# Performance work log

Measured on AMD Instinct MI355X. Metric: run time of the kernel, lower is better.

## Reference

```python
import jax, jax.numpy as jnp
import numpy as np


def setup_inputs() -> dict:
    key0 = jax.random.key(0)
    kq, kk, kv = jax.random.split(key0, 3)
    B, S, E = 4, 2048, 1024
    query = jax.random.normal(kq, (B, S, E), dtype=jnp.float32)
    key = jax.random.normal(kk, (B, S, E), dtype=jnp.float32)
    value = jax.random.normal(kv, (B, S, E), dtype=jnp.float32)
    attn_mask = jnp.zeros((B, S, S), dtype=jnp.float32)
    return {"query": query, "key": key, "value": value, "attn_mask": attn_mask}


def reference(query, key, value, attn_mask):
    # qk = Q K^T / sqrt(E) + mask; softmax over last dim; dropout is
    # identity in eval mode (reference baseline); out = attn @ V.
    E = query.shape[-1]
    scale = 1.0 / jnp.sqrt(jnp.asarray(E, dtype=query.dtype))
    qk = jnp.einsum("bqe,bke->bqk", query, key) * scale + attn_mask
    attn = jax.nn.softmax(qk, axis=-1)
    out = jnp.einsum("bqk,bke->bqe", attn, value)
    return out
```

## Files before the change

kernel.cpp:

```cpp
#include <hip/hip_runtime.h>
#include <stdint.h>
#include <math.h>

typedef unsigned short u16;
typedef short bf16x8 __attribute__((ext_vector_type(8)));
typedef unsigned short u16x8 __attribute__((ext_vector_type(8)));
typedef unsigned short u16x4 __attribute__((ext_vector_type(4)));
typedef float f32x4 __attribute__((ext_vector_type(4)));

typedef __attribute__((address_space(1))) const void gvoid;
typedef __attribute__((address_space(3))) void lvoid;

#define LOG2E 1.4426950408889634f

__device__ __forceinline__ float bf2f(u16 u) {
  union { unsigned int i; float f; } v; v.i = ((unsigned int)u) << 16; return v.f;
}
__device__ __forceinline__ u16 f2bf(float f) {
  union { float ff; unsigned int i; } v; v.ff = f;
  unsigned int x = v.i;
  return (u16)((x + 0x7FFFu + ((x >> 16) & 1u)) >> 16);
}

__global__ __launch_bounds__(256)
void cvt2_f32_bf16(const float* __restrict__ s0, u16* __restrict__ d0,
                   const float* __restrict__ s1, u16* __restrict__ d1, long n)
{
  const long nb = n / 2048;
  const float* src = (blockIdx.x < nb) ? s0 : s1;
  u16* dst         = (blockIdx.x < nb) ? d0 : d1;
  const long bid   = (blockIdx.x < nb) ? blockIdx.x : (blockIdx.x - nb);
  long i = (bid * 256 + threadIdx.x) * 8;
  if (i + 8 > n) return;
  f32x4 a = *(const f32x4*)&src[i];
  f32x4 b = *(const f32x4*)&src[i + 4];
  u16x8 o;
#pragma unroll
  for (int j = 0; j < 4; j++) { o[j] = f2bf(a[j]); o[4 + j] = f2bf(b[j]); }
  *(u16x8*)&dst[i] = o;
}

__global__ __launch_bounds__(256)
void cvt_f32_bf16(const float* __restrict__ src, u16* __restrict__ dst, long n)
{
  long i = ((long)blockIdx.x * 256 + threadIdx.x) * 8;
  if (i + 8 > n) return;
  f32x4 a = *(const f32x4*)&src[i];
  f32x4 b = *(const f32x4*)&src[i + 4];
  u16x8 o;
#pragma unroll
  for (int j = 0; j < 4; j++) { o[j] = f2bf(a[j]); o[4 + j] = f2bf(b[j]); }
  *(u16x8*)&dst[i] = o;
}

__global__ __launch_bounds__(256)
void transcvt_v(const float* __restrict__ V, u16* __restrict__ VT, int S, int E)
{
  __shared__ u16 t[64][72];
  const int b = blockIdx.z;
  const float* Vb = V + (long)b * S * E;
  u16* VTb = VT + (long)b * S * E;
  const int k0 = blockIdx.x * 64, n0 = blockIdx.y * 64;
  const int tid = threadIdx.x;
#pragma unroll
  for (int p = 0; p < 2; p++) {
    int kk = p * 32 + (tid >> 3);
    int nn = (tid & 7) * 8;
    f32x4 a = *(const f32x4*)&Vb[(long)(k0 + kk) * E + n0 + nn];
    f32x4 c = *(const f32x4*)&Vb[(long)(k0 + kk) * E + n0 + nn + 4];
#pragma unroll
    for (int j = 0; j < 4; j++) { t[nn + j][kk] = f2bf(a[j]); t[nn + 4 + j][kk] = f2bf(c[j]); }
  }
  __syncthreads();
#pragma unroll
  for (int p = 0; p < 2; p++) {
    int nn = p * 32 + (tid >> 3);
    int kk = (tid & 7) * 8;
    u16x8 u;
#pragma unroll
    for (int j = 0; j < 8; j++) u[j] = t[nn][kk + j];
    *(u16x8*)&VTb[(long)(n0 + nn) * S + k0 + kk] = u;
  }
}

template<int HASMASK, int COUT>
__global__ __launch_bounds__(256, 3)
void gemm_bt_fast(const u16* __restrict__ A, int lda, long aRowOff,
                  const u16* __restrict__ B, int ldb, long bBatchStride,
                  void* __restrict__ Cp, int ldc, long cRowOff,
                  const float* __restrict__ maskf,
                  int K, float scale, long g0, int S)
{
  const int tid  = threadIdx.x;
  const int lane = tid & 63;
  const int wave = tid >> 6;
  const long gTile = g0 + (long)blockIdx.y * 128;
  const int  bidx  = (int)(gTile / S);
  const int  nTile = blockIdx.x * 128;

  __shared__ u16 As[128][32];
  __shared__ u16 Bs[128][32];

  const u16* Ab = A + (gTile - aRowOff) * (long)lda;
  const u16* Bb = B + (long)bidx * bBatchStride + (long)nTile * ldb;

  const int qm = (wave >> 1) * 64;
  const int qn = (wave & 1) * 64;
  const int lm  = lane & 15;
  const int lkB = (lane >> 4) * 16;

  const int sr = lane >> 2;
  const int sc = (lane & 3) * 8;

  f32x4 acc[4][4];
#pragma unroll
  for (int i = 0; i < 4; i++)
#pragma unroll
    for (int j = 0; j < 4; j++) acc[i][j] = (f32x4){0.f, 0.f, 0.f, 0.f};

  for (int k0 = 0; k0 < K; k0 += 32) {
#pragma unroll
    for (int p = 0; p < 2; p++) {
      const int chunk = wave * 2 + p;
      const int r = chunk * 16 + sr;
      __builtin_amdgcn_global_load_lds(
          (gvoid*)&Ab[(long)r * lda + k0 + sc],
          (lvoid*)((char*)&As[0][0] + chunk * 1024),
          16, 0, 0);
      __builtin_amdgcn_global_load_lds(
          (gvoid*)&Bb[(long)r * ldb + k0 + sc],
          (lvoid*)((char*)&Bs[0][0] + chunk * 1024),
          16, 0, 0);
    }
    __syncthreads();

    bf16x8 af[4], bfr[4];
#pragma unroll
    for (int rt = 0; rt < 4; rt++)
      af[rt] = *(const bf16x8*)((const char*)&As[qm + rt * 16 + lm][0] + lkB);
#pragma unroll
    for (int ct = 0; ct < 4; ct++)
      bfr[ct] = *(const bf16x8*)((const char*)&Bs[qn + ct * 16 + lm][0] + lkB);

#pragma unroll
    for (int rt = 0; rt < 4; rt++)
#pragma unroll
      for (int ct = 0; ct < 4; ct++)
        acc[rt][ct] = __builtin_amdgcn_mfma_f32_16x16x32_bf16(af[rt], bfr[ct], acc[rt][ct], 0, 0, 0);
    __syncthreads();
  }

  const int lr = (lane >> 4) * 4;
#pragma unroll
  for (int rt = 0; rt < 4; rt++) {
#pragma unroll
    for (int ct = 0; ct < 4; ct++) {
      long gr = gTile + qm + rt * 16 + lr;
      int  cc = nTile + qn + ct * 16 + lm;
#pragma unroll
      for (int i = 0; i < 4; i++) {
        float v = acc[rt][ct][i] * scale;
        if (HASMASK) v += maskf[(gr + i) * (long)ldc + cc];
        if (COUT == 0)
          ((u16*)Cp)[(gr + i - cRowOff) * (long)ldc + cc] = f2bf(v);
        else
          ((float*)Cp)[(gr + i - cRowOff) * (long)ldc + cc] = v;
      }
    }
  }
}

template<int ASRC, int BSRC, int BMODE, int HASMASK, int COUT>
__global__ __launch_bounds__(256, 2)
void gemm_bt(const void* __restrict__ Ap, int lda, long aRowOff,
             const void* __restrict__ Bp, int ldb, long bBatchStride,
             void* __restrict__ Cp, int ldc, long cRowOff,
             const float* __restrict__ maskf,
             int K, float scale, long g0, int S)
{
  const int tid  = threadIdx.x;
  const int lane = tid & 63;
  const int wave = tid >> 6;
  const long gTile = g0 + (long)blockIdx.y * 128;
  const int  b     = (int)(gTile / S);
  const int  nTile = blockIdx.x * 128;

  __shared__ u16 As[128][40];
  __shared__ u16 Bs[128][40];

  const int qm = (wave >> 1) * 64;
  const int qn = (wave & 1) * 64;

  f32x4 acc[4][4];
#pragma unroll
  for (int i = 0; i < 4; i++)
#pragma unroll
    for (int j = 0; j < 4; j++) acc[i][j] = (f32x4){0.f, 0.f, 0.f, 0.f};

  const u16*   Ab = (const u16*)Ap   + (gTile - aRowOff) * (long)lda;
  const float* Af = (const float*)Ap + (gTile - aRowOff) * (long)lda;
  const u16*   Bb = (const u16*)Bp   + (long)b * bBatchStride;
  const float* Bf = (const float*)Bp + (long)b * bBatchStride;

  const int lm = lane & 15;
  const int lk = (lane >> 4) * 8;

  for (int k0 = 0; k0 < K; k0 += 32) {
    if (ASRC == 0) {
      int srow = tid >> 2, scol = (tid & 3) * 8;
#pragma unroll
      for (int p = 0; p < 2; p++) {
        int r = p * 64 + srow;
        *(u16x8*)&As[r][scol] = *(const u16x8*)&Ab[(long)r * lda + k0 + scol];
      }
    } else {
      int srow = tid >> 3, scol = (tid & 7) * 4;
#pragma unroll
      for (int p = 0; p < 4; p++) {
        int r = p * 32 + srow;
        f32x4 a = *(const f32x4*)&Af[(long)r * lda + k0 + scol];
        u16x4 o;
#pragma unroll
        for (int j = 0; j < 4; j++) o[j] = f2bf(a[j]);
        *(u16x4*)&As[r][scol] = o;
      }
    }
    if (BMODE == 0) {
      if (BSRC == 0) {
        int srow = tid >> 2, scol = (tid & 3) * 8;
#pragma unroll
        for (int p = 0; p < 2; p++) {
          int r = p * 64 + srow;
          *(u16x8*)&Bs[r][scol] = *(const u16x8*)&Bb[(long)(nTile + r) * ldb + k0 + scol];
        }
      } else {
        int srow = tid >> 3, scol = (tid & 7) * 4;
#pragma unroll
        for (int p = 0; p < 4; p++) {
          int r = p * 32 + srow;
          f32x4 a = *(const f32x4*)&Bf[(long)(nTile + r) * ldb + k0 + scol];
          u16x4 o;
#pragma unroll
          for (int j = 0; j < 4; j++) o[j] = f2bf(a[j]);
          *(u16x4*)&Bs[r][scol] = o;
        }
      }
    }
    __syncthreads();

    bf16x8 af[4], bfr[4];
#pragma unroll
    for (int rt = 0; rt < 4; rt++)
      af[rt] = *(const bf16x8*)&As[qm + rt * 16 + lm][lk];
    if (BMODE == 0) {
#pragma unroll
      for (int ct = 0; ct < 4; ct++)
        bfr[ct] = *(const bf16x8*)&Bs[qn + ct * 16 + lm][lk];
    } else {
#pragma unroll
      for (int ct = 0; ct < 4; ct++) {
        const float* vp = Bf + (long)(k0 + lk) * ldb + nTile + qn + ct * 16 + lm;
#pragma unroll
        for (int j = 0; j < 8; j++) bfr[ct][j] = (short)f2bf(vp[(long)j * ldb]);
      }
    }
#pragma unroll
    for (int rt = 0; rt < 4; rt++)
#pragma unroll
      for (int ct = 0; ct < 4; ct++)
        acc[rt][ct] = __builtin_amdgcn_mfma_f32_16x16x32_bf16(af[rt], bfr[ct], acc[rt][ct], 0, 0, 0);
    __syncthreads();
  }

  const int lr = (lane >> 4) * 4;
#pragma unroll
  for (int rt = 0; rt < 4; rt++) {
#pragma unroll
    for (int ct = 0; ct < 4; ct++) {
      long gr = gTile + qm + rt * 16 + lr;
      int  cc = nTile + qn + ct * 16 + lm;
#pragma unroll
      for (int i = 0; i < 4; i++) {
        float v = acc[rt][ct][i] * scale;
        if (HASMASK) v += maskf[(gr + i) * (long)ldc + cc];
        if (COUT == 0)
          ((u16*)Cp)[(gr + i - cRowOff) * (long)ldc + cc] = f2bf(v);
        else
          ((float*)Cp)[(gr + i - cRowOff) * (long)ldc + cc] = v;
      }
    }
  }
}

template<int HASM>
__global__ __launch_bounds__(256)
void softmax_rows(u16* __restrict__ Sbuf, const float* __restrict__ maskf, int ncols)
{
  const long row = blockIdx.x;
  u16* rp = Sbuf + row * (long)ncols;
  const int tid = threadIdx.x;

  u16x8 u = *(const u16x8*)&rp[tid * 8];
  float x[8];
  if (HASM) {
    const float* mp = maskf + row * (long)ncols + tid * 8;
    f32x4 ma = *(const f32x4*)&mp[0];
    f32x4 mb = *(const f32x4*)&mp[4];
#pragma unroll
    for (int i = 0; i < 4; i++) { x[i] = bf2f(u[i]) + ma[i]; x[4 + i] = bf2f(u[4 + i]) + mb[i]; }
  } else {
#pragma unroll
    for (int i = 0; i < 8; i++) x[i] = bf2f(u[i]);
  }
  float m = -3.0e38f;
#pragma unroll
  for (int i = 0; i < 8; i++) m = fmaxf(m, x[i]);
#pragma unroll
  for (int off = 32; off; off >>= 1) m = fmaxf(m, __shfl_xor(m, off, 64));
  __shared__ float redm[4];
  if ((tid & 63) == 0) redm[tid >> 6] = m;
  __syncthreads();
  m = fmaxf(fmaxf(redm[0], redm[1]), fmaxf(redm[2], redm[3]));

  float e[8];
  float s = 0.f;
#pragma unroll
  for (int i = 0; i < 8; i++) { e[i] = exp2f((x[i] - m) * LOG2E); s += e[i]; }
#pragma unroll
  for (int off = 32; off; off >>= 1) s += __shfl_xor(s, off, 64);
  __shared__ float reds[4];
  if ((tid & 63) == 0) reds[tid >> 6] = s;
  __syncthreads();
  s = reds[0] + reds[1] + reds[2] + reds[3];

  float inv = 1.0f / s;
  u16x8 o;
#pragma unroll
  for (int i = 0; i < 8; i++) o[i] = f2bf(e[i] * inv);
  *(u16x8*)&rp[tid * 8] = o;
}

extern "C" void kernel_launch(void* const* d_in, const int* in_sizes, int n_in,
                              void* d_out, int out_size, void* d_ws, size_t ws_size,
                              hipStream_t stream)
{
  const float* Q    = (const float*)d_in[0];
  const float* Km   = (const float*)d_in[1];
  const float* V    = (const float*)d_in[2];
  const float* mask = (const float*)d_in[3];
  float* out = (float*)d_out;

  const long qsz = in_sizes[0];
  const long msz = in_sizes[3];
  const long E = 1024;
  const long S = (msz / qsz) * E;
  const long B = qsz / (S * E);
  const long G = B * S;
  const float scale = 1.0f / sqrtf((float)E);

  const size_t mergedBytes = (size_t)(2 * qsz) * 2 + (size_t)G * S * 2;
  if (ws_size >= mergedBytes) {
    char* w = (char*)d_ws;
    u16* Qb   = (u16*)w;
    u16* Kb   = (u16*)(w + (size_t)qsz * 2);
    u16* Sbuf = (u16*)(w + (size_t)(2 * qsz) * 2);
    u16* VTb  = Qb;

    cvt2_f32_bf16<<<dim3((unsigned)(2 * qsz / 2048)), 256, 0, stream>>>(
        Q, Qb, Km, Kb, qsz);

    gemm_bt_fast<0, 0><<<dim3(S / 128, G / 128), 256, 0, stream>>>(
        Qb, (int)E, 0L, Kb, (int)E, S * E,
        Sbuf, (int)S, 0L, nullptr, (int)E, scale, 0L, (int)S);

    softmax_rows<1><<<dim3((unsigned)G), 256, 0, stream>>>(Sbuf, mask, (int)S);

    transcvt_v<<<dim3(S / 64, E / 64, B), 256, 0, stream>>>(V, VTb, (int)S, (int)E);

    gemm_bt_fast<0, 1><<<dim3(E / 128, G / 128), 256, 0, stream>>>(
        Sbuf, (int)S, 0L, VTb, (int)S, E * S,
        out, (int)E, 0L, nullptr, (int)S, 1.0f, 0L, (int)S);
    return;
  }

  const size_t convBytes = (size_t)(3 * qsz) * 2;
  const size_t rowBytes  = (size_t)S * 2;
  char* w = (char*)d_ws;
  size_t avail = ws_size;
  const bool haveConv = (ws_size >= convBytes + 128 * rowBytes);

  u16 *Qb = nullptr, *Kb = nullptr, *VTb = nullptr;
  if (haveConv) {
    Qb  = (u16*)w;              w += (size_t)qsz * 2;
    Kb  = (u16*)w;              w += (size_t)qsz * 2;
    VTb = (u16*)w;              w += (size_t)qsz * 2;
    avail -= convBytes;
  }
  long Rmax = (long)((avail / rowBytes) / 128) * 128;
  if (Rmax > G) Rmax = G;
  if (Rmax < 128) Rmax = 128;
  u16* Sbuf = (u16*)w;

  if (haveConv) {
    cvt_f32_bf16<<<dim3((unsigned)(qsz / 2048)), 256, 0, stream>>>(Q, Qb, qsz);
    cvt_f32_bf16<<<dim3((unsigned)(qsz / 2048)), 256, 0, stream>>>(Km, Kb, qsz);
    transcvt_v<<<dim3(S / 64, E / 64, B), 256, 0, stream>>>(V, VTb, (int)S, (int)E);
  }

  for (long g0 = 0; g0 < G; g0 += Rmax) {
    const long R = (G - g0 < Rmax) ? (G - g0) : Rmax;
    if (haveConv) {
      gemm_bt_fast<1, 0><<<dim3(S / 128, R / 128), 256, 0, stream>>>(
          Qb, (int)E, 0L, Kb, (int)E, S * E,
          Sbuf, (int)S, g0, mask, (int)E, scale, g0, (int)S);
    } else {
      gemm_bt<1, 1, 0, 1, 0><<<dim3(S / 128, R / 128), 256, 0, stream>>>(
          Q, (int)E, 0L, Km, (int)E, S * E,
          Sbuf, (int)S, g0, mask, (int)E, scale, g0, (int)S);
    }
    softmax_rows<0><<<dim3(R), 256, 0, stream>>>(Sbuf, nullptr, (int)S);
    if (haveConv) {
      gemm_bt_fast<0, 1><<<dim3(E / 128, R / 128), 256, 0, stream>>>(
          Sbuf, (int)S, g0, VTb, (int)S, E * S,
          out, (int)E, 0L, nullptr, (int)S, 1.0f, g0, (int)S);
    } else {
      gemm_bt<0, 1, 1, 0, 1><<<dim3(E / 128, R / 128), 256, 0, stream>>>(
          Sbuf, (int)S, g0, V, (int)E, S * E,
          out, (int)E, 0L, nullptr, (int)S, 1.0f, g0, (int)S);
    }
  }
}
```

Baseline: 279.2 us.

## Double-buffer LDS tiles in gemm_bt_fast to overlap global loads with MFMA

```diff
diff --git a/kernel.cpp b/kernel.cpp
--- a/kernel.cpp
+++ b/kernel.cpp
@@ -98,8 +98,8 @@
   const int  bidx  = (int)(gTile / S);
   const int  nTile = blockIdx.x * 128;
 
-  __shared__ u16 As[128][32];
-  __shared__ u16 Bs[128][32];
+  __shared__ u16 As[2][128][32];
+  __shared__ u16 Bs[2][128][32];
 
   const u16* Ab = A + (gTile - aRowOff) * (long)lda;
   const u16* Bb = B + (long)bidx * bBatchStride + (long)nTile * ldb;
@@ -107,7 +107,7 @@
   const int qm = (wave >> 1) * 64;
   const int qn = (wave & 1) * 64;
   const int lm  = lane & 15;
-  const int lkB = (lane >> 4) * 16;
+  const int lk8 = (lane >> 4) * 8;
 
   const int sr = lane >> 2;
   const int sc = (lane & 3) * 8;
@@ -118,36 +118,56 @@
 #pragma unroll
     for (int j = 0; j < 4; j++) acc[i][j] = (f32x4){0.f, 0.f, 0.f, 0.f};
 
-  for (int k0 = 0; k0 < K; k0 += 32) {
+  auto STAGE = [&](int buf, int t) {
 #pragma unroll
     for (int p = 0; p < 2; p++) {
       const int chunk = wave * 2 + p;
-      const int r = chunk * 16 + sr;
+      const int rr = chunk * 16 + sr;
+      const int gc = t * 32 + sc;
       __builtin_amdgcn_global_load_lds(
-          (gvoid*)&Ab[(long)r * lda + k0 + sc],
-          (lvoid*)((char*)&As[0][0] + chunk * 1024),
+          (gvoid*)&Ab[(long)rr * lda + gc],
+          (lvoid*)((char*)&As[buf][0][0] + chunk * 1024),
           16, 0, 0);
       __builtin_amdgcn_global_load_lds(
-          (gvoid*)&Bb[(long)r * ldb + k0 + sc],
-          (lvoid*)((char*)&Bs[0][0] + chunk * 1024),
+          (gvoid*)&Bb[(long)rr * ldb + gc],
+          (lvoid*)((char*)&Bs[buf][0][0] + chunk * 1024),
           16, 0, 0);
     }
-    __syncthreads();
-
+  };
+
+  auto COMPUTE = [&](int buf) {
     bf16x8 af[4], bfr[4];
 #pragma unroll
     for (int rt = 0; rt < 4; rt++)
-      af[rt] = *(const bf16x8*)((const char*)&As[qm + rt * 16 + lm][0] + lkB);
+      af[rt] = *(const bf16x8*)&As[buf][qm + rt * 16 + lm][lk8];
 #pragma unroll
     for (int ct = 0; ct < 4; ct++)
-      bfr[ct] = *(const bf16x8*)((const char*)&Bs[qn + ct * 16 + lm][0] + lkB);
-
+      bfr[ct] = *(const bf16x8*)&Bs[buf][qn + ct * 16 + lm][lk8];
 #pragma unroll
     for (int rt = 0; rt < 4; rt++)
 #pragma unroll
       for (int ct = 0; ct < 4; ct++)
         acc[rt][ct] = __builtin_amdgcn_mfma_f32_16x16x32_bf16(af[rt], bfr[ct], acc[rt][ct], 0, 0, 0);
-    __syncthreads();
+  };
+
+  const int nt = K >> 5;
+  STAGE(0, 0);
+  int cur = 0;
+  for (int t = 0; t < nt; t++) {
+    if (t + 1 < nt) {
+      STAGE(cur ^ 1, t + 1);
+      asm volatile("s_waitcnt vmcnt(4)" ::: "memory");
+    } else {
+      asm volatile("s_waitcnt vmcnt(0)" ::: "memory");
+    }
+    __builtin_amdgcn_sched_barrier(0);
+    __builtin_amdgcn_s_barrier();
+    __builtin_amdgcn_sched_barrier(0);
+    COMPUTE(cur);
+    __builtin_amdgcn_sched_barrier(0);
+    __builtin_amdgcn_s_barrier();
+    __builtin_amdgcn_sched_barrier(0);
+    cur ^= 1;
   }
 
   const int lr = (lane >> 4) * 4;
```

Result: no change. 282.4 us (+1.1%).

## Add 256x256 tiled QK^T GEMM with direct-to-LDS loads and phased MFMA schedule

Applied to the files above, without the earlier changes.

```diff
diff --git a/kernel.cpp b/kernel.cpp
--- a/kernel.cpp
+++ b/kernel.cpp
@@ -81,6 +81,181 @@
     for (int j = 0; j < 8; j++) u[j] = t[nn][kk + j];
     *(u16x8*)&VTb[(long)(n0 + nn) * S + k0 + kk] = u;
   }
+}
+
+__global__ __launch_bounds__(512, 1)
+void gemm_bt_256(const u16* __restrict__ A, int lda,
+                 const u16* __restrict__ B, int ldb, long bBatchStride,
+                 u16* __restrict__ C, int ldc,
+                 int K, float scale, int S)
+{
+  __shared__ u16 LA[2][256][64];
+  __shared__ u16 LB[2][256][64];
+
+  const int tid  = threadIdx.x;
+  const int lane = tid & 63;
+  const int wave = tid >> 6;
+  const int wm   = wave >> 2;
+  const int wn   = wave & 3;
+  const long gTile = (long)blockIdx.y * 256;
+  const int  bidx  = (int)(gTile / S);
+  const int  nTile = blockIdx.x * 256;
+
+  const u16* Ab = A + gTile * (long)lda;
+  const u16* Bb = B + (long)bidx * bBatchStride + (long)nTile * ldb;
+
+  const int lm  = lane & 15;
+  const int lkc = (lane >> 4) * 8;
+  const int srw = lane >> 3;
+  const int scg = (lane & 7) * 8;
+
+  f32x4 acc[8][4];
+#pragma unroll
+  for (int i = 0; i < 8; i++)
+#pragma unroll
+    for (int j = 0; j < 4; j++) acc[i][j] = (f32x4){0.f, 0.f, 0.f, 0.f};
+
+  bf16x8 afr[8], bA[4], bB[4];
+
+#define STG_A(buf, T, h)                                                      \
+  {                                                                           \
+    _Pragma("unroll")                                                         \
+    for (int p_ = 0; p_ < 2; p_++) {                                          \
+      const int ch_ = wave * 2 + p_;                                          \
+      const int rr_ = (h) * 128 + ch_ * 8 + srw;                              \
+      __builtin_amdgcn_global_load_lds(                                       \
+          (gvoid*)&Ab[(long)rr_ * lda + (T) * 64 + scg],                      \
+          (lvoid*)((char*)&LA[0][0][0] + (buf) * 32768 + (h) * 16384 + ch_ * 1024), \
+          16, 0, 0);                                                          \
+    }                                                                         \
+  }
+#define STG_B(buf, T, h)                                                      \
+  {                                                                           \
+    _Pragma("unroll")                                                         \
+    for (int p_ = 0; p_ < 2; p_++) {                                          \
+      const int ch_ = wave * 2 + p_;                                          \
+      const int rr_ = (h) * 128 + ch_ * 8 + srw;                              \
+      __builtin_amdgcn_global_load_lds(                                       \
+          (gvoid*)&Bb[(long)rr_ * ldb + (T) * 64 + scg],                      \
+          (lvoid*)((char*)&LB[0][0][0] + (buf) * 32768 + (h) * 16384 + ch_ * 1024), \
+          16, 0, 0);                                                          \
+    }                                                                         \
+  }
+
+#define LDA_HALF(buf, mh)                                                     \
+  {                                                                           \
+    _Pragma("unroll")                                                         \
+    for (int m_ = 0; m_ < 4; m_++)                                            \
+      _Pragma("unroll")                                                       \
+      for (int kk_ = 0; kk_ < 2; kk_++)                                       \
+        afr[m_ * 2 + kk_] = *(const bf16x8*)&LA[buf][wm * 128 + ((mh) * 4 + m_) * 16 + lm][kk_ * 32 + lkc]; \
+  }
+#define LDB_HALF(buf, nh, dst)                                                \
+  {                                                                           \
+    _Pragma("unroll")                                                         \
+    for (int n_ = 0; n_ < 2; n_++)                                            \
+      _Pragma("unroll")                                                       \
+      for (int kk_ = 0; kk_ < 2; kk_++)                                       \
+        dst[n_ * 2 + kk_] = *(const bf16x8*)&LB[buf][wn * 64 + ((nh) * 2 + n_) * 16 + lm][kk_ * 32 + lkc]; \
+  }
+
+#define PH(mh, nh, bp)                                                        \
+  {                                                                           \
+    __builtin_amdgcn_sched_barrier(0);                                        \
+    __builtin_amdgcn_s_barrier();                                             \
+    asm volatile("s_waitcnt lgkmcnt(0)" ::: "memory");                        \
+    __builtin_amdgcn_sched_barrier(0);                                        \
+    __builtin_amdgcn_s_setprio(1);                                            \
+    _Pragma("unroll")                                                         \
+    for (int m_ = 0; m_ < 4; m_++)                                            \
+      _Pragma("unroll")                                                       \
+      for (int n_ = 0; n_ < 2; n_++)                                          \
+        _Pragma("unroll")                                                     \
+        for (int kk_ = 0; kk_ < 2; kk_++)                                     \
+          acc[(mh) * 4 + m_][(nh) * 2 + n_] =                                 \
+              __builtin_amdgcn_mfma_f32_16x16x32_bf16(                        \
+                  afr[m_ * 2 + kk_], bp[n_ * 2 + kk_],                        \
+                  acc[(mh) * 4 + m_][(nh) * 2 + n_], 0, 0, 0);                \
+    __builtin_amdgcn_s_setprio(0);                                            \
+    __builtin_amdgcn_sched_barrier(0);                                        \
+    __builtin_amdgcn_s_barrier();                                             \
+  }
+
+  const int NT = K >> 6;
+  const int NI = NT >> 1;
+
+  STG_A(0, 0, 0); STG_A(0, 0, 1); STG_B(0, 0, 0); STG_B(0, 0, 1);
+  STG_A(1, 1, 0); STG_B(1, 1, 0);
+  asm volatile("s_waitcnt vmcnt(0)" ::: "memory");
+  __builtin_amdgcn_sched_barrier(0);
+  __builtin_amdgcn_s_barrier();
+
+  for (int i = 0; i < NI - 1; i++) {
+    const int t0 = 2 * i, t1 = t0 + 1;
+    LDA_HALF(0, 0); LDB_HALF(0, 0, bA);
+    STG_B(1, t1, 1);
+    PH(0, 0, bA);
+    LDB_HALF(0, 1, bB);
+    STG_A(1, t1, 1);
+    PH(0, 1, bB);
+    LDA_HALF(0, 1);
+    STG_A(0, t0 + 2, 0);
+    PH(1, 0, bA);
+    STG_B(0, t0 + 2, 0);
+    asm volatile("s_waitcnt vmcnt(4)" ::: "memory");
+    PH(1, 1, bB);
+    LDA_HALF(1, 0); LDB_HALF(1, 0, bA);
+    STG_B(0, t0 + 2, 1);
+    PH(0, 0, bA);
+    LDB_HALF(1, 1, bB);
+    STG_A(0, t0 + 2, 1);
+    PH(0, 1, bB);
+    LDA_HALF(1, 1);
+    STG_A(1, t1 + 2, 0);
+    PH(1, 0, bA);
+    STG_B(1, t1 + 2, 0);
+    asm volatile("s_waitcnt vmcnt(4)" ::: "memory");
+    PH(1, 1, bB);
+  }
+
+  {
+    const int t1 = NT - 1;
+    LDA_HALF(0, 0); LDB_HALF(0, 0, bA);
+    STG_B(1, t1, 1);
+    PH(0, 0, bA);
+    LDB_HALF(0, 1, bB);
+    STG_A(1, t1, 1);
+    PH(0, 1, bB);
+    LDA_HALF(0, 1);
+    PH(1, 0, bA);
+    asm volatile("s_waitcnt vmcnt(0)" ::: "memory");
+    PH(1, 1, bB);
+    LDA_HALF(1, 0); LDB_HALF(1, 0, bA);
+    PH(0, 0, bA);
+    LDB_HALF(1, 1, bB);
+    PH(0, 1, bB);
+    LDA_HALF(1, 1);
+    PH(1, 0, bA);
+    PH(1, 1, bB);
+  }
+
+  const int lr = (lane >> 4) * 4;
+#pragma unroll
+  for (int mf = 0; mf < 8; mf++) {
+#pragma unroll
+    for (int nf = 0; nf < 4; nf++) {
+      long gr = gTile + wm * 128 + mf * 16 + lr;
+      int  cc = nTile + wn * 64 + nf * 16 + lm;
+#pragma unroll
+      for (int i2 = 0; i2 < 4; i2++)
+        C[(gr + i2) * (long)ldc + cc] = f2bf(acc[mf][nf][i2] * scale);
+    }
+  }
+#undef STG_A
+#undef STG_B
+#undef LDA_HALF
+#undef LDB_HALF
+#undef PH
 }
 
 template<int HASMASK, int COUT>
@@ -359,7 +534,7 @@
   const float scale = 1.0f / sqrtf((float)E);
 
   const size_t mergedBytes = (size_t)(2 * qsz) * 2 + (size_t)G * S * 2;
-  if (ws_size >= mergedBytes) {
+  if (ws_size >= mergedBytes && (S % 256) == 0 && (G % 256) == 0) {
     char* w = (char*)d_ws;
     u16* Qb   = (u16*)w;
     u16* Kb   = (u16*)(w + (size_t)qsz * 2);
@@ -369,9 +544,9 @@
     cvt2_f32_bf16<<<dim3((unsigned)(2 * qsz / 2048)), 256, 0, stream>>>(
         Q, Qb, Km, Kb, qsz);
 
-    gemm_bt_fast<0, 0><<<dim3(S / 128, G / 128), 256, 0, stream>>>(
-        Qb, (int)E, 0L, Kb, (int)E, S * E,
-        Sbuf, (int)S, 0L, nullptr, (int)E, scale, 0L, (int)S);
+    gemm_bt_256<<<dim3(S / 256, G / 256), 512, 0, stream>>>(
+        Qb, (int)E, Kb, (int)E, S * E,
+        Sbuf, (int)S, (int)E, scale, (int)S);
 
     softmax_rows<1><<<dim3((unsigned)G), 256, 0, stream>>>(Sbuf, mask, (int)S);
 
```

Result: slower. 286.1 us (+2.4%).
